# Kernel tuning notes

Hardware: AMD Instinct MI355X
Metric: run time of the kernel (lower is better)

The kernel has to match this reference:

```python
import jax, jax.numpy as jnp
import numpy as np

N_NODES = 100000
D_FEAT = 128
N_EDGES = 640000


def setup_inputs() -> dict:
    key = jax.random.key(0)
    k1, k2, k3 = jax.random.split(key, 3)
    node_features = jax.random.normal(k1, (N_NODES, D_FEAT), dtype=jnp.float32)
    edge_index = jax.random.randint(k2, (2, N_EDGES), 0, N_NODES, dtype=jnp.int64)
    # Linear(2*d, 1): weight stored as [2d, 1] (input-major), bias [1]
    W = jax.random.normal(k3, (2 * D_FEAT, 1), dtype=jnp.float32) / np.sqrt(2 * D_FEAT)
    b = jnp.zeros((1,), dtype=jnp.float32)
    return {"node_features": node_features, "edge_index": edge_index, "W": W, "b": b}


def reference(node_features, edge_index, W, b):
    # Gather source/target node features per edge: [E, d] each
    src = node_features[edge_index[0]]
    dst = node_features[edge_index[1]]
    d = node_features.shape[1]
    # cat([src, dst]) @ W == src @ W[:d] + dst @ W[d:] (avoids materializing [E, 2d])
    logits = src @ W[:d] + dst @ W[d:] + b  # [E, 1]
    return jax.nn.sigmoid(logits)
```

## Files before the change

### kernel.cpp

```cpp
#include <hip/hip_runtime.h>
#include <math.h>

#define N_NODES 100000
#define D_FEAT  128
#define N_EDGES 640000

#define ROWS_PER_CHUNK 16
#define N_CHUNKS (N_NODES / ROWS_PER_CHUNK)
#define K1_WPB   4
#define K1_BLOCK (K1_WPB * 64)
#define K1_GRID  782

__global__ __launch_bounds__(K1_BLOCK) void node_dots_kernel(
    const float* __restrict__ feat, const float* __restrict__ W,
    float* __restrict__ a, float* __restrict__ c)
{
    __shared__ float4 lds[K1_WPB][ROWS_PER_CHUNK][33];

    const int wave  = threadIdx.x >> 6;
    const int lane  = threadIdx.x & 63;
    const int gwave = blockIdx.x * K1_WPB + wave;
    const int nwav  = gridDim.x * K1_WPB;

    const int r = lane & 15;
    const int q = lane >> 4;

    float4 w0[8], w1[8];
    #pragma unroll
    for (int j = 0; j < 8; ++j) {
        w0[j] = *reinterpret_cast<const float4*>(W + q * 32 + j * 4);
        w1[j] = *reinterpret_cast<const float4*>(W + D_FEAT + q * 32 + j * 4);
    }

    for (int ch = gwave; ch < N_CHUNKS; ch += nwav) {
        const size_t base = (size_t)ch * ROWS_PER_CHUNK * D_FEAT;

        float4 st[8];
        #pragma unroll
        for (int k = 0; k < 8; ++k) {
            const int g = k * 64 + lane;
            st[k] = *reinterpret_cast<const float4*>(feat + base + (size_t)g * 4);
        }
        #pragma unroll
        for (int k = 0; k < 8; ++k) {
            const int g = k * 64 + lane;
            lds[wave][g >> 5][g & 31] = st[k];
        }

        float pa = 0.f, pc = 0.f;
        #pragma unroll
        for (int j = 0; j < 8; ++j) {
            const float4 f = lds[wave][r][q * 8 + j];
            pa += f.x * w0[j].x + f.y * w0[j].y + f.z * w0[j].z + f.w * w0[j].w;
            pc += f.x * w1[j].x + f.y * w1[j].y + f.z * w1[j].z + f.w * w1[j].w;
        }

        pa += __shfl_down(pa, 16, 64);
        pc += __shfl_down(pc, 16, 64);
        pa += __shfl_down(pa, 32, 64);
        pc += __shfl_down(pc, 32, 64);

        if (lane < 16) {
            const int n = ch * ROWS_PER_CHUNK + r;
            a[n] = pa;
            c[n] = pc;
        }
    }
}

__global__ void edge_kernel(const int* __restrict__ ei,
                            const float* __restrict__ a,
                            const float* __restrict__ c,
                            const float* __restrict__ b,
                            float* __restrict__ out)
{
    const int t = blockIdx.x * blockDim.x + threadIdx.x;
    const int e0 = t * 4;
    if (e0 >= N_EDGES) return;

    const float bb = b[0];
    const int4 s = *reinterpret_cast<const int4*>(ei + e0);
    const int4 d = *reinterpret_cast<const int4*>(ei + N_EDGES + e0);

    float4 o;
    o.x = 1.0f / (1.0f + __expf(-(a[s.x] + c[d.x] + bb)));
    o.y = 1.0f / (1.0f + __expf(-(a[s.y] + c[d.y] + bb)));
    o.z = 1.0f / (1.0f + __expf(-(a[s.z] + c[d.z] + bb)));
    o.w = 1.0f / (1.0f + __expf(-(a[s.w] + c[d.w] + bb)));

    *reinterpret_cast<float4*>(out + e0) = o;
}

extern "C" void kernel_launch(void* const* d_in, const int* in_sizes, int n_in,
                              void* d_out, int out_size, void* d_ws, size_t ws_size,
                              hipStream_t stream)
{
    const float* feat = (const float*)d_in[0];
    const int*   ei   = (const int*)d_in[1];
    const float* W    = (const float*)d_in[2];
    const float* b    = (const float*)d_in[3];
    float*       out  = (float*)d_out;

    float* a = (float*)d_ws;
    float* c = a + N_NODES;

    node_dots_kernel<<<K1_GRID, K1_BLOCK, 0, stream>>>(feat, W, a, c);

    const int nthreads = N_EDGES / 4;
    const int nblk2 = (nthreads + 255) / 256;
    edge_kernel<<<nblk2, 256, 0, stream>>>(ei, a, c, b, out);
}
```

Before: 22.99 us.

## Drop LDS staging in node dot kernel, fold bias into a, nontemporal edge stores

```diff
diff --git a/kernel.cpp b/kernel.cpp
--- a/kernel.cpp
+++ b/kernel.cpp
@@ -5,90 +5,77 @@
 #define D_FEAT  128
 #define N_EDGES 640000
 
-#define ROWS_PER_CHUNK 16
-#define N_CHUNKS (N_NODES / ROWS_PER_CHUNK)
-#define K1_WPB   4
-#define K1_BLOCK (K1_WPB * 64)
-#define K1_GRID  782
+typedef float nfloat4 __attribute__((ext_vector_type(4)));
 
-__global__ __launch_bounds__(K1_BLOCK) void node_dots_kernel(
+__global__ __launch_bounds__(256) void node_dots_kernel(
     const float* __restrict__ feat, const float* __restrict__ W,
+    const float* __restrict__ bias,
     float* __restrict__ a, float* __restrict__ c)
 {
-    __shared__ float4 lds[K1_WPB][ROWS_PER_CHUNK][33];
+    const int lane32 = threadIdx.x & 31;
+    const int grp    = (blockIdx.x * blockDim.x + threadIdx.x) >> 5;
+    const int ngrp   = (gridDim.x * blockDim.x) >> 5;
 
-    const int wave  = threadIdx.x >> 6;
-    const int lane  = threadIdx.x & 63;
-    const int gwave = blockIdx.x * K1_WPB + wave;
-    const int nwav  = gridDim.x * K1_WPB;
+    const float4 w0 = *reinterpret_cast<const float4*>(W + lane32 * 4);
+    const float4 w1 = *reinterpret_cast<const float4*>(W + D_FEAT + lane32 * 4);
+    const float bb = bias[0];
 
-    const int r = lane & 15;
-    const int q = lane >> 4;
-
-    float4 w0[8], w1[8];
-    #pragma unroll
-    for (int j = 0; j < 8; ++j) {
-        w0[j] = *reinterpret_cast<const float4*>(W + q * 32 + j * 4);
-        w1[j] = *reinterpret_cast<const float4*>(W + D_FEAT + q * 32 + j * 4);
-    }
-
-    for (int ch = gwave; ch < N_CHUNKS; ch += nwav) {
-        const size_t base = (size_t)ch * ROWS_PER_CHUNK * D_FEAT;
-
-        float4 st[8];
+    for (int n0 = grp * 4; n0 < N_NODES; n0 += ngrp * 4) {
+        float4 f[4];
         #pragma unroll
-        for (int k = 0; k < 8; ++k) {
-            const int g = k * 64 + lane;
-            st[k] = *reinterpret_cast<const float4*>(feat + base + (size_t)g * 4);
-        }
-        #pragma unroll
-        for (int k = 0; k < 8; ++k) {
-            const int g = k * 64 + lane;
-            lds[wave][g >> 5][g & 31] = st[k];
+        for (int j = 0; j < 4; ++j) {
+            f[j] = *reinterpret_cast<const float4*>(
+                feat + (size_t)(n0 + j) * D_FEAT + lane32 * 4);
         }
 
-        float pa = 0.f, pc = 0.f;
+        float pa[4], pc[4];
         #pragma unroll
-        for (int j = 0; j < 8; ++j) {
-            const float4 f = lds[wave][r][q * 8 + j];
-            pa += f.x * w0[j].x + f.y * w0[j].y + f.z * w0[j].z + f.w * w0[j].w;
-            pc += f.x * w1[j].x + f.y * w1[j].y + f.z * w1[j].z + f.w * w1[j].w;
+        for (int j = 0; j < 4; ++j) {
+            pa[j] = f[j].x * w0.x + f[j].y * w0.y + f[j].z * w0.z + f[j].w * w0.w;
+            pc[j] = f[j].x * w1.x + f[j].y * w1.y + f[j].z * w1.z + f[j].w * w1.w;
         }
 
-        pa += __shfl_down(pa, 16, 64);
-        pc += __shfl_down(pc, 16, 64);
-        pa += __shfl_down(pa, 32, 64);
-        pc += __shfl_down(pc, 32, 64);
+        #pragma unroll
+        for (int off = 16; off > 0; off >>= 1) {
+            #pragma unroll
+            for (int j = 0; j < 4; ++j) {
+                pa[j] += __shfl_down(pa[j], off, 32);
+                pc[j] += __shfl_down(pc[j], off, 32);
+            }
+        }
 
-        if (lane < 16) {
-            const int n = ch * ROWS_PER_CHUNK + r;
-            a[n] = pa;
-            c[n] = pc;
+        if (lane32 == 0) {
+            #pragma unroll
+            for (int j = 0; j < 4; ++j) {
+                a[n0 + j] = pa[j] + bb;
+                c[n0 + j] = pc[j];
+            }
         }
     }
 }
 
-__global__ void edge_kernel(const int* __restrict__ ei,
-                            const float* __restrict__ a,
-                            const float* __restrict__ c,
-                            const float* __restrict__ b,
-                            float* __restrict__ out)
+__global__ __launch_bounds__(256) void edge_kernel(
+    const int* __restrict__ ei,
+    const float* __restrict__ a, const float* __restrict__ c,
+    float* __restrict__ out)
 {
     const int t = blockIdx.x * blockDim.x + threadIdx.x;
     const int e0 = t * 4;
     if (e0 >= N_EDGES) return;
 
-    const float bb = b[0];
     const int4 s = *reinterpret_cast<const int4*>(ei + e0);
     const int4 d = *reinterpret_cast<const int4*>(ei + N_EDGES + e0);
 
-    float4 o;
-    o.x = 1.0f / (1.0f + __expf(-(a[s.x] + c[d.x] + bb)));
-    o.y = 1.0f / (1.0f + __expf(-(a[s.y] + c[d.y] + bb)));
-    o.z = 1.0f / (1.0f + __expf(-(a[s.z] + c[d.z] + bb)));
-    o.w = 1.0f / (1.0f + __expf(-(a[s.w] + c[d.w] + bb)));
+    const float as0 = a[s.x], as1 = a[s.y], as2 = a[s.z], as3 = a[s.w];
+    const float cd0 = c[d.x], cd1 = c[d.y], cd2 = c[d.z], cd3 = c[d.w];
 
-    *reinterpret_cast<float4*>(out + e0) = o;
+    nfloat4 o;
+    o.x = 1.0f / (1.0f + __expf(-(as0 + cd0)));
+    o.y = 1.0f / (1.0f + __expf(-(as1 + cd1)));
+    o.z = 1.0f / (1.0f + __expf(-(as2 + cd2)));
+    o.w = 1.0f / (1.0f + __expf(-(as3 + cd3)));
+
+    __builtin_nontemporal_store(o, reinterpret_cast<nfloat4*>(out + e0));
 }
 
 extern "C" void kernel_launch(void* const* d_in, const int* in_sizes, int n_in,
@@ -104,9 +91,9 @@
     float* a = (float*)d_ws;
     float* c = a + N_NODES;
 
-    node_dots_kernel<<<K1_GRID, K1_BLOCK, 0, stream>>>(feat, W, a, c);
+    node_dots_kernel<<<2048, 256, 0, stream>>>(feat, W, b, a, c);
 
     const int nthreads = N_EDGES / 4;
     const int nblk2 = (nthreads + 255) / 256;
-    edge_kernel<<<nblk2, 256, 0, stream>>>(ei, a, c, b, out);
+    edge_kernel<<<nblk2, 256, 0, stream>>>(ei, a, c, out);
 }
```

After: 22.69 us. No clear change (-1.3%).
